# Optimization experiments

Hardware: AMD Instinct MI355X
Metric: run time of the kernel (lower is better)

Reference implementation:

```python
import jax, jax.numpy as jnp
import numpy as np

S, B, H, NH = 2048, 2, 1024, 16
DH = H // NH

def setup_inputs() -> dict:
    key = jax.random.key(0)
    ks = jax.random.split(key, 4)
    x = jax.random.normal(ks[0], (S, B, H), dtype=jnp.float32)
    attention_mask = jnp.ones((B, 1, S, S), dtype=bool)
    rotary_pos_emb = jax.random.uniform(ks[1], (S, 1, 1, DH), dtype=jnp.float32)
    Wqkv = jax.random.normal(ks[2], (H, 3 * H), dtype=jnp.float32) * (1.0 / np.sqrt(H))
    bqkv = jnp.zeros((3 * H,), dtype=jnp.float32)
    Wproj = jax.random.normal(ks[3], (H, H), dtype=jnp.float32) * (1.0 / np.sqrt(H))
    bproj = jnp.zeros((H,), dtype=jnp.float32)
    return {"x": x, "attention_mask": attention_mask, "rotary_pos_emb": rotary_pos_emb,
            "Wqkv": Wqkv, "bqkv": bqkv, "Wproj": Wproj, "bproj": bproj}

def reference(x, attention_mask, rotary_pos_emb, Wqkv, bqkv, Wproj, bproj):
    s, b, h = x.shape
    dh = h // NH
    # QKV projection; per-head layout [s,b,NH,3*dh] then split (matches view+chunk)
    qkv = (x @ Wqkv + bqkv).reshape(s, b, NH, 3 * dh)
    q, k, v = jnp.split(qkv, 3, axis=-1)  # each [s,b,NH,dh]
    # RoPE (non-interleaved, rot_dim == head_dim)
    cos = jnp.cos(rotary_pos_emb)  # [s,1,1,dh]
    sin = jnp.sin(rotary_pos_emb)
    def rope(t):
        t1, t2 = jnp.split(t, 2, axis=-1)
        return t * cos + jnp.concatenate((-t2, t1), axis=-1) * sin
    q = rope(q)
    k = rope(k)
    scale = 1.0 / np.sqrt(dh).astype(np.float32)
    # scores: [b,NH,t,s]
    scores = jnp.einsum('tbhd,sbhd->bhts', q, k) * scale
    scores = jnp.where(attention_mask, scores, jnp.float32(-1e9))
    attn = jax.nn.softmax(scores, axis=-1)
    out = jnp.einsum('bhts,sbhd->tbhd', attn, v).reshape(s, b, h)
    return out @ Wproj + bproj
```

## Files before the change

### kernel.cpp

```cpp
#include <hip/hip_runtime.h>
#include <hip/hip_bf16.h>

typedef __attribute__((ext_vector_type(8))) short bf16x8;
typedef __attribute__((ext_vector_type(4))) float f32x4;
typedef __attribute__((ext_vector_type(16))) float f32x16;
typedef __attribute__((ext_vector_type(4))) unsigned short u16x4;

#define S_LEN 2048
#define BATCH 2
#define NHEAD 16
#define DHEAD 64
#define HD    1024
#define MROWS 4096
#define NQKV  3072
#define NBH   32
#define KSPLIT 2
#define KSEG  (S_LEN / KSPLIT)


static __device__ __forceinline__ unsigned short f2bf(float f) {
  union { float f; unsigned u; } v; v.f = f;
  unsigned r = v.u + 0x7FFFu + ((v.u >> 16) & 1u);
  return (unsigned short)(r >> 16);
}
static __device__ __forceinline__ float bf2f(unsigned short h) {
  union { unsigned u; float f; } v; v.u = ((unsigned)h) << 16;
  return v.f;
}
static __device__ __forceinline__ unsigned cvt_pk(float a, float b) {
  unsigned r;
  asm("v_cvt_pk_bf16_f32 %0, %1, %2" : "=v"(r) : "v"(a), "v"(b));
  return r;
}
static __device__ __forceinline__ float exp2_hw(float x) {
  float r;
  asm("v_exp_f32 %0, %1" : "=v"(r) : "v"(x));
  return r;
}

static __device__ __forceinline__ void gl_lds16(const void* g, void* l) {
  __builtin_amdgcn_global_load_lds(
      (__attribute__((address_space(1))) void*)g,
      (__attribute__((address_space(3))) void*)l, 16, 0, 0);
}


static __device__ __forceinline__ void cvt_body(const float* __restrict__ x,
                                                unsigned short* __restrict__ Xfm,
                                                int mt, int kp, char* lmem) {
  float (*ltile)[36] = reinterpret_cast<float(*)[36]>(lmem);
  int t = threadIdx.x;
  int r = t >> 3, c4 = t & 7;
  const float* src = x + (size_t)(mt * 64 + r) * HD + kp * 32 + c4 * 4;
  float4 v0 = *reinterpret_cast<const float4*>(src);
  float4 v1 = *reinterpret_cast<const float4*>(src + (size_t)32 * HD);
  *reinterpret_cast<float4*>(&ltile[r][c4 * 4]) = v0;
  *reinterpret_cast<float4*>(&ltile[r + 32][c4 * 4]) = v1;
  __syncthreads();
  int rowin = ((t >> 6) << 4) + (t & 15), ch = (t >> 4) & 3;
  bf16x8 o;
#pragma unroll
  for (int e = 0; e < 8; ++e) o[e] = (short)f2bf(ltile[rowin][ch * 8 + e]);
  *reinterpret_cast<bf16x8*>(Xfm + (((size_t)mt * 32 + kp) * 256 + t) * 8) = o;
}

static __device__ __forceinline__ void transw_body(const float* __restrict__ W,
                                                   unsigned short* __restrict__ Wt,
                                                   int K, int N, int nt, int kb,
                                                   char* lmem) {
  unsigned short (*tile)[72] = reinterpret_cast<unsigned short(*)[72]>(lmem);
  int n0 = nt * 64, k0 = kb * 64;
  int t = threadIdx.x;
  int r  = t >> 2;
  int c4 = (t & 3) * 16;
  const float* src = W + (size_t)(k0 + r) * N + n0 + c4;
#pragma unroll
  for (int j = 0; j < 16; j += 4) {
    float4 v = *reinterpret_cast<const float4*>(src + j);
    tile[r][c4 + j + 0] = f2bf(v.x);
    tile[r][c4 + j + 1] = f2bf(v.y);
    tile[r][c4 + j + 2] = f2bf(v.z);
    tile[r][c4 + j + 3] = f2bf(v.w);
  }
  __syncthreads();
  int rowin = ((t >> 6) << 4) + (t & 15), ch = (t >> 4) & 3;
  int KP = K >> 5;
#pragma unroll
  for (int p = 0; p < 2; ++p) {
    bf16x8 o;
#pragma unroll
    for (int e = 0; e < 8; ++e) o[e] = (short)tile[p * 32 + ch * 8 + e][rowin];
    *reinterpret_cast<bf16x8*>(Wt + (((size_t)nt * KP + (k0 >> 5) + p) * 256 + t) * 8) = o;
  }
}

__global__ void k_prep(const float* __restrict__ x, unsigned short* __restrict__ Xfm,
                       const float* __restrict__ Wq, unsigned short* __restrict__ Wqt,
                       const float* __restrict__ Wp, unsigned short* __restrict__ Wpt) {
  __shared__ __align__(16) char lmem[9216];
  int id = blockIdx.x;
  if (id < 768) {
    transw_body(Wq, Wqt, HD, NQKV, id % 48, id / 48, lmem);
  } else if (id < 1024) {
    int j = id - 768;
    transw_body(Wp, Wpt, HD, HD, j % 16, j / 16, lmem);
  } else {
    int j = id - 1024;
    cvt_body(x, Xfm, j >> 5, j & 31, lmem);
  }
}

template <int OUT_BF16, int BN>
__global__ void __launch_bounds__(256)
k_gemm(const unsigned short* __restrict__ A, const unsigned short* __restrict__ Bt,
       const float* __restrict__ bias, void* __restrict__ Cout, int M, int N, int K) {
  constexpr int NF = BN / 32;
  __shared__ unsigned short As[128 * 32];
  __shared__ unsigned short Bs[BN * 32];
  int t = threadIdx.x;
  int lane = t & 63;
  int w = t >> 6;
  int g = lane >> 4, i = lane & 15;
  int wr = w >> 1, wc = w & 1;
  int bx = blockIdx.x, by = blockIdx.y;

  f32x4 acc[4][NF] = {};

  const size_t tstride = (size_t)K * 64;
  const unsigned short* a_s0 = A  + (size_t)(2 * by) * tstride + t * 8;
  const unsigned short* a_s1 = a_s0 + tstride;
  const unsigned short* b_s0 = Bt + (size_t)(bx * (BN / 64)) * tstride + t * 8;
  const unsigned short* b_s1 = b_s0 + tstride;
  unsigned short* a_d0 = &As[t * 8];
  unsigned short* a_d1 = &As[(256 + t) * 8];
  unsigned short* b_d0 = &Bs[t * 8];
  unsigned short* b_d1 = &Bs[(256 + t) * 8];

  for (int kt = 0; kt < K; kt += 32) {
    size_t koff = (size_t)kt * 64;
    __syncthreads();
    gl_lds16(a_s0 + koff, a_d0);
    gl_lds16(a_s1 + koff, a_d1);
    gl_lds16(b_s0 + koff, b_d0);
    if constexpr (BN == 128) gl_lds16(b_s1 + koff, b_d1);
    __syncthreads();

    bf16x8 af[4], bf[NF];
#pragma unroll
    for (int m = 0; m < 4; ++m)
      af[m] = *reinterpret_cast<const bf16x8*>(&As[(wr * 256 + m * 64 + lane) * 8]);
#pragma unroll
    for (int n = 0; n < NF; ++n)
      bf[n] = *reinterpret_cast<const bf16x8*>(&Bs[((wc * NF + n) * 64 + lane) * 8]);
#pragma unroll
    for (int m = 0; m < 4; ++m)
#pragma unroll
      for (int n = 0; n < NF; ++n)
        acc[m][n] = __builtin_amdgcn_mfma_f32_16x16x32_bf16(af[m], bf[n], acc[m][n], 0, 0, 0);
  }

  int crow0 = by * 128 + wr * 64;
  int ccol0 = bx * BN + wc * (BN / 2);
#pragma unroll
  for (int n = 0; n < NF; ++n) {
    int col = ccol0 + n * 16 + i;
    float bv = bias[col];
#pragma unroll
    for (int m = 0; m < 4; ++m) {
#pragma unroll
      for (int r = 0; r < 4; ++r) {
        int row = crow0 + m * 16 + g * 4 + r;
        float v = acc[m][n][r] + bv;
        if (OUT_BF16)
          reinterpret_cast<unsigned short*>(Cout)[(size_t)row * N + col] = f2bf(v);
        else
          reinterpret_cast<float*>(Cout)[(size_t)row * N + col] = v;
      }
    }
  }
}

__global__ void k_rope(const unsigned short* __restrict__ QKV, const float* __restrict__ rot,
                       unsigned short* __restrict__ Qg, unsigned short* __restrict__ Kg,
                       unsigned short* __restrict__ Vg) {
  __shared__ unsigned short vtile[32][72];
  int s0 = blockIdx.x * 32;
  int bh = blockIdx.y;
  int b = bh >> 4, nh = bh & 15;
  int t = threadIdx.x;
  int c  = t & 31;
  int hi = (t >> 5) & 1;
  int ks = t >> 6;
  int d0 = ks * 16 + hi * 8;
  int s = s0 + c;
  const unsigned short* base = QKV + ((size_t)s * BATCH + b) * NQKV + nh * 192;

  float cs[8], sn[8];
#pragma unroll
  for (int j = 0; j < 8; j += 4) {
    float4 rv = *reinterpret_cast<const float4*>(rot + (size_t)s * DHEAD + d0 + j);
    cs[j + 0] = cosf(rv.x); sn[j + 0] = sinf(rv.x);
    cs[j + 1] = cosf(rv.y); sn[j + 1] = sinf(rv.y);
    cs[j + 2] = cosf(rv.z); sn[j + 2] = sinf(rv.z);
    cs[j + 3] = cosf(rv.w); sn[j + 3] = sinf(rv.w);
  }
  float sgn = (d0 < 32) ? -1.f : 1.f;
  bf16x8 qv = *reinterpret_cast<const bf16x8*>(base + d0);
  bf16x8 qp = *reinterpret_cast<const bf16x8*>(base + (d0 ^ 32));
  bf16x8 kv = *reinterpret_cast<const bf16x8*>(base + 64 + d0);
  bf16x8 kp = *reinterpret_cast<const bf16x8*>(base + 64 + (d0 ^ 32));
  bf16x8 qo, ko;
#pragma unroll
  for (int j = 0; j < 8; ++j) {
    float q = bf2f((unsigned short)qv[j]) * cs[j] + sgn * bf2f((unsigned short)qp[j]) * sn[j];
    float k = bf2f((unsigned short)kv[j]) * cs[j] + sgn * bf2f((unsigned short)kp[j]) * sn[j];
    qo[j] = (short)f2bf(q * 0.18033688f);
    ko[j] = (short)f2bf(k);
  }
  size_t blk = ((size_t)bh * (S_LEN / 32) + (s0 >> 5)) * 2048;
  *reinterpret_cast<bf16x8*>(Qg + blk + t * 8) = qo;
  *reinterpret_cast<bf16x8*>(Kg + blk + t * 8) = ko;

  bf16x8 vv = *reinterpret_cast<const bf16x8*>(base + 128 + d0);
  *reinterpret_cast<bf16x8*>(&vtile[c][d0]) = vv;
  __syncthreads();
  int vbr = t >> 7, h = (t >> 6) & 1, hi2 = (t >> 5) & 1, cc = t & 31;
  int d = 32 * h + cc;
  bf16x8 vo;
#pragma unroll
  for (int j = 0; j < 8; ++j) vo[j] = (short)vtile[vbr * 16 + hi2 * 8 + j][d];
  size_t vblk = ((size_t)bh * (S_LEN / 16) + (s0 >> 4) + vbr) * 1024;
  *reinterpret_cast<bf16x8*>(Vg + vblk + (t & 127) * 8) = vo;
}


static __device__ __forceinline__ void sm_pv(const f32x16& sc, const bf16x8* vfr,
                                             float& l_acc, f32x16& o0, f32x16& o1) {
  float p[16];
#pragma unroll
  for (int r = 0; r < 16; ++r) p[r] = exp2_hw(sc[r]);
  float s0 = (p[0] + p[1]) + (p[2] + p[3]);
  float s1 = (p[4] + p[5]) + (p[6] + p[7]);
  float s2 = (p[8] + p[9]) + (p[10] + p[11]);
  float s3 = (p[12] + p[13]) + (p[14] + p[15]);
  l_acc += (s0 + s1) + (s2 + s3);
#pragma unroll
  for (int ksl = 0; ksl < 2; ++ksl) {
    unsigned A0 = cvt_pk(p[8 * ksl + 0], p[8 * ksl + 1]);
    unsigned A1 = cvt_pk(p[8 * ksl + 2], p[8 * ksl + 3]);
    unsigned A2 = cvt_pk(p[8 * ksl + 4], p[8 * ksl + 5]);
    unsigned A3 = cvt_pk(p[8 * ksl + 6], p[8 * ksl + 7]);
    asm volatile("v_permlane32_swap_b32 %0, %1" : "+v"(A0), "+v"(A2));
    asm volatile("v_permlane32_swap_b32 %0, %1" : "+v"(A1), "+v"(A3));
    union { unsigned u[4]; bf16x8 v; } pa;
    pa.u[0] = A0; pa.u[1] = A1; pa.u[2] = A2; pa.u[3] = A3;
    __builtin_amdgcn_s_setprio(1);
    o0 = __builtin_amdgcn_mfma_f32_32x32x16_bf16(pa.v, vfr[2 * ksl + 0], o0, 0, 0, 0);
    o1 = __builtin_amdgcn_mfma_f32_32x32x16_bf16(pa.v, vfr[2 * ksl + 1], o1, 0, 0, 0);
    __builtin_amdgcn_s_setprio(0);
  }
}

__global__ void __launch_bounds__(256, 2)
k_flash(const unsigned short* __restrict__ Qg, const unsigned short* __restrict__ Kg,
        const unsigned short* __restrict__ Vg, unsigned short* __restrict__ Opart,
        float* __restrict__ Lpart) {
  __shared__ unsigned short kv_lds[2 * 8192];
  int bh = blockIdx.x, qt = blockIdx.y, kv = blockIdx.z;
  int t = threadIdx.x, lane = t & 63;
  int c = lane & 31, hi = lane >> 5;

  int q0 = qt * 128 + (t >> 6) * 32;
  int kv0 = kv * KSEG;
  const unsigned short* Qb = Qg + (size_t)bh * S_LEN * DHEAD + (size_t)q0 * DHEAD;
  const unsigned short* Kb = Kg + (size_t)bh * S_LEN * DHEAD;
  const unsigned short* Vb = Vg + (size_t)bh * S_LEN * DHEAD;

  bf16x8 qf[4];
#pragma unroll
  for (int ks = 0; ks < 4; ++ks)
    qf[ks] = *reinterpret_cast<const bf16x8*>(Qb + ((size_t)ks * 64 + lane) * 8);

#define STAGE(kt, bufi) do {                                                   \
    const unsigned short* _ks = Kb + (size_t)(kt) * DHEAD;                     \
    const unsigned short* _vs = Vb + (size_t)(kt) * DHEAD;                     \
    unsigned short* _kd = &kv_lds[(bufi) * 8192];                              \
    unsigned short* _vd = _kd + 4096;                                          \
    gl_lds16(_ks + t * 8, _kd + t * 8);                                        \
    gl_lds16(_ks + (t + 256) * 8, _kd + (t + 256) * 8);                        \
    gl_lds16(_vs + t * 8, _vd + t * 8);                                        \
    gl_lds16(_vs + (t + 256) * 8, _vd + (t + 256) * 8);                        \
  } while (0)

  f32x16 o0 = {}, o1 = {};
  float l_acc = 0.f;
  int cur = 0;

  STAGE(kv0, 0);
  for (int kt = kv0; kt < kv0 + KSEG; kt += 64) {
    __syncthreads();
    int nxt = kv0 + (((kt - kv0) + 64) & (KSEG - 1));
    STAGE(nxt, cur ^ 1);

    const unsigned short* kbuf = &kv_lds[cur * 8192];
    const unsigned short* vbuf = kbuf + 4096;

    f32x16 scA = {}, scB = {};
    __builtin_amdgcn_s_setprio(1);
#pragma unroll
    for (int ks = 0; ks < 4; ++ks) {
      bf16x8 kf = *reinterpret_cast<const bf16x8*>(kbuf + (ks * 64 + lane) * 8);
      scA = __builtin_amdgcn_mfma_f32_32x32x16_bf16(kf, qf[ks], scA, 0, 0, 0);
    }
#pragma unroll
    for (int ks = 0; ks < 4; ++ks) {
      bf16x8 kf = *reinterpret_cast<const bf16x8*>(kbuf + (256 + ks * 64 + lane) * 8);
      scB = __builtin_amdgcn_mfma_f32_32x32x16_bf16(kf, qf[ks], scB, 0, 0, 0);
    }
    __builtin_amdgcn_s_setprio(0);

    bf16x8 va[4], vb[4];
#pragma unroll
    for (int g = 0; g < 2; ++g) {
      va[2 * g + 0] = *reinterpret_cast<const bf16x8*>(vbuf + (g * 128 + lane) * 8);
      va[2 * g + 1] = *reinterpret_cast<const bf16x8*>(vbuf + (g * 128 + 64 + lane) * 8);
      vb[2 * g + 0] = *reinterpret_cast<const bf16x8*>(vbuf + ((g + 2) * 128 + lane) * 8);
      vb[2 * g + 1] = *reinterpret_cast<const bf16x8*>(vbuf + ((g + 2) * 128 + 64 + lane) * 8);
    }

    sm_pv(scA, va, l_acc, o0, o1);
    sm_pv(scB, vb, l_acc, o0, o1);
    cur ^= 1;
  }
#undef STAGE

  float l_tot = l_acc + __shfl_xor(l_acc, 32, 64);

  unsigned short* Op = Opart + ((size_t)kv * NBH + bh) * S_LEN * DHEAD;
  if (hi == 0) Lpart[((size_t)kv * NBH + bh) * S_LEN + q0 + c] = l_tot;
#pragma unroll
  for (int r = 0; r < 16; ++r) {
    int crow = (r & 3) + 8 * (r >> 2) + 4 * hi;
    size_t rowoff = (size_t)(q0 + crow) * DHEAD;
    Op[rowoff + c]      = f2bf(o0[r]);
    Op[rowoff + 32 + c] = f2bf(o1[r]);
  }
}

__global__ void k_reduce(const unsigned short* __restrict__ Op, const float* __restrict__ Lp,
                         unsigned short* __restrict__ Afm) {
  __shared__ unsigned short lds[64][72];
  const int kvO = NBH * S_LEN * DHEAD;
  const int kvL = NBH * S_LEN;
  int mt = blockIdx.x, nh = blockIdx.y;
  int t = threadIdx.x;
  int lq = (t >> 3) & 31, gd = t & 7;
  int qg = mt * 32 + lq;

  bf16x8 gr[4];
#pragma unroll
  for (int kvb = 0; kvb < 4; ++kvb) {
    int kv = kvb >> 1, b = kvb & 1;
    gr[kvb] = *reinterpret_cast<const bf16x8*>(
        Op + (size_t)kv * kvO + ((size_t)(b * 16 + nh) * S_LEN + qg) * DHEAD + gd * 8);
  }
#pragma unroll
  for (int b = 0; b < 2; ++b) {
    size_t li = (size_t)(b * 16 + nh) * S_LEN + qg;
    float inv = 1.0f / (Lp[li] + Lp[kvL + li]);
    bf16x8 o;
#pragma unroll
    for (int e = 0; e < 8; ++e)
      o[e] = (short)f2bf((bf2f((unsigned short)gr[b][e]) +
                          bf2f((unsigned short)gr[2 + b][e])) * inv);
    *reinterpret_cast<bf16x8*>(&lds[b * 32 + lq][gd * 8]) = o;
  }
  __syncthreads();

  int rowin = ((t >> 6) << 4) + (t & 15), ch = (t >> 4) & 3;
  int lr = (rowin & 1) * 32 + (rowin >> 1);
#pragma unroll
  for (int p = 0; p < 2; ++p) {
    bf16x8 o = *reinterpret_cast<const bf16x8*>(&lds[lr][p * 32 + ch * 8]);
    *reinterpret_cast<bf16x8*>(Afm + (((size_t)mt * 32 + nh * 2 + p) * 256 + t) * 8) = o;
  }
}

extern "C" void kernel_launch(void* const* d_in, const int* in_sizes, int n_in,
                              void* d_out, int out_size, void* d_ws, size_t ws_size,
                              hipStream_t stream) {
  const float* x     = (const float*)d_in[0];
  const float* rot   = (const float*)d_in[2];
  const float* Wqkv  = (const float*)d_in[3];
  const float* bqkv  = (const float*)d_in[4];
  const float* Wproj = (const float*)d_in[5];
  const float* bproj = (const float*)d_in[6];
  float* out = (float*)d_out;

  char* ws = (char*)d_ws;
  unsigned short* xb   = (unsigned short*)(ws);
  unsigned short* Wqt  = (unsigned short*)(ws + 8388608);
  unsigned short* Wpt  = (unsigned short*)(ws + 14680064);
  unsigned short* QKV  = (unsigned short*)(ws + 16777216);
  unsigned short* Qs   = (unsigned short*)(ws + 41943040);
  unsigned short* Kst  = (unsigned short*)(ws + 50331648);
  unsigned short* Vtt  = (unsigned short*)(ws + 58720256);
  unsigned short* Opart = (unsigned short*)(ws + 16777216);
  float*          Lpart = (float*)(ws + 33554432);
  unsigned short* attn  = xb;

  k_prep<<<3072, 256, 0, stream>>>(x, xb, Wqkv, Wqt, Wproj, Wpt);
  k_gemm<1, 128><<<dim3(NQKV / 128, MROWS / 128), 256, 0, stream>>>(xb, Wqt, bqkv, QKV,
                                                                    MROWS, NQKV, HD);
  k_rope<<<dim3(S_LEN / 32, BATCH * NHEAD), 256, 0, stream>>>(QKV, rot, Qs, Kst, Vtt);
  k_flash<<<dim3(NBH, S_LEN / 128, KSPLIT), 256, 0, stream>>>(Qs, Kst, Vtt, Opart, Lpart);
  k_reduce<<<dim3(MROWS / 64, NHEAD), 256, 0, stream>>>(Opart, Lpart, attn);
  k_gemm<0, 64><<<dim3(HD / 64, MROWS / 128), 256, 0, stream>>>(attn, Wpt, bproj, out,
                                                                MROWS, HD, HD);
}
```

Before: 129.1 us.

## Fuse split-KV reduction into output projection GEMM A-tile load

Removes the separate k_reduce kernel and has the output projection GEMM combine the two KV-split partial outputs and normalize by the summed softmax denominators while loading each A tile into LDS. This saves one kernel launch and the round trip of the combined attention tensor through global memory. In exchange, each of the 16 column blocks recomputes the reduction for its row tile, the A loads become register-staged instead of direct-to-LDS, and the new GEMM has no visible software pipelining, which may cost compute efficiency.

```diff
diff --git a/kernel.cpp b/kernel.cpp
--- a/kernel.cpp
+++ b/kernel.cpp
@@ -43,7 +43,6 @@
       (__attribute__((address_space(1))) void*)g,
       (__attribute__((address_space(3))) void*)l, 16, 0, 0);
 }
-
 
 static __device__ __forceinline__ void cvt_body(const float* __restrict__ x,
                                                 unsigned short* __restrict__ Xfm,
@@ -180,6 +179,97 @@
   }
 }
 
+__global__ void __launch_bounds__(256)
+k_gemm2f(const unsigned short* __restrict__ Op, const float* __restrict__ Lp,
+         const unsigned short* __restrict__ Bt, const float* __restrict__ bias,
+         float* __restrict__ Cout) {
+  constexpr int K = HD, N = HD;
+  const int kvO = NBH * S_LEN * DHEAD;
+  const int kvL = NBH * S_LEN;
+  __shared__ unsigned short As[128 * 32];
+  __shared__ unsigned short Bs[64 * 32];
+  int t = threadIdx.x;
+  int lane = t & 63;
+  int w = t >> 6;
+  int g = lane >> 4, i = lane & 15;
+  int wr = w >> 1, wc = w & 1;
+  int bx = blockIdx.x, by = blockIdx.y;
+
+  f32x4 acc[4][2] = {};
+
+  const size_t tstride = (size_t)K * 64;
+  const unsigned short* b_s0 = Bt + (size_t)bx * tstride + t * 8;
+
+  int rowin = ((t >> 6) << 4) + (t & 15);
+  int ch = (t >> 4) & 3;
+  int r0 = by * 128 + rowin;
+  int r1 = r0 + 64;
+  int q0 = r0 >> 1, b0 = r0 & 1;
+  int q1 = r1 >> 1, b1 = r1 & 1;
+
+  for (int kt = 0; kt < K; kt += 32) {
+    size_t koff = (size_t)kt * 64;
+    __syncthreads();
+    gl_lds16(b_s0 + koff, &Bs[t * 8]);
+    int nh = kt >> 6;
+    int d = (kt & 63) + ch * 8;
+    {
+      size_t li = (size_t)(b0 * 16 + nh) * S_LEN + q0;
+      float inv = 1.0f / (Lp[li] + Lp[kvL + li]);
+      bf16x8 g0 = *reinterpret_cast<const bf16x8*>(Op + li * DHEAD + d);
+      bf16x8 g1 = *reinterpret_cast<const bf16x8*>(Op + (size_t)kvO + li * DHEAD + d);
+      bf16x8 o;
+#pragma unroll
+      for (int e = 0; e < 8; ++e)
+        o[e] = (short)f2bf((bf2f((unsigned short)g0[e]) +
+                            bf2f((unsigned short)g1[e])) * inv);
+      *reinterpret_cast<bf16x8*>(&As[t * 8]) = o;
+    }
+    {
+      size_t li = (size_t)(b1 * 16 + nh) * S_LEN + q1;
+      float inv = 1.0f / (Lp[li] + Lp[kvL + li]);
+      bf16x8 g0 = *reinterpret_cast<const bf16x8*>(Op + li * DHEAD + d);
+      bf16x8 g1 = *reinterpret_cast<const bf16x8*>(Op + (size_t)kvO + li * DHEAD + d);
+      bf16x8 o;
+#pragma unroll
+      for (int e = 0; e < 8; ++e)
+        o[e] = (short)f2bf((bf2f((unsigned short)g0[e]) +
+                            bf2f((unsigned short)g1[e])) * inv);
+      *reinterpret_cast<bf16x8*>(&As[(256 + t) * 8]) = o;
+    }
+    __syncthreads();
+
+    bf16x8 af[4], bf[2];
+#pragma unroll
+    for (int m = 0; m < 4; ++m)
+      af[m] = *reinterpret_cast<const bf16x8*>(&As[(wr * 256 + m * 64 + lane) * 8]);
+#pragma unroll
+    for (int n = 0; n < 2; ++n)
+      bf[n] = *reinterpret_cast<const bf16x8*>(&Bs[((wc * 2 + n) * 64 + lane) * 8]);
+#pragma unroll
+    for (int m = 0; m < 4; ++m)
+#pragma unroll
+      for (int n = 0; n < 2; ++n)
+        acc[m][n] = __builtin_amdgcn_mfma_f32_16x16x32_bf16(af[m], bf[n], acc[m][n], 0, 0, 0);
+  }
+
+  int crow0 = by * 128 + wr * 64;
+  int ccol0 = bx * 64 + wc * 32;
+#pragma unroll
+  for (int n = 0; n < 2; ++n) {
+    int col = ccol0 + n * 16 + i;
+    float bv = bias[col];
+#pragma unroll
+    for (int m = 0; m < 4; ++m) {
+#pragma unroll
+      for (int r = 0; r < 4; ++r) {
+        int row = crow0 + m * 16 + g * 4 + r;
+        Cout[(size_t)row * N + col] = acc[m][n][r] + bv;
+      }
+    }
+  }
+}
+
 __global__ void k_rope(const unsigned short* __restrict__ QKV, const float* __restrict__ rot,
                        unsigned short* __restrict__ Qg, unsigned short* __restrict__ Kg,
                        unsigned short* __restrict__ Vg) {
@@ -233,7 +323,6 @@
   *reinterpret_cast<bf16x8*>(Vg + vblk + (t & 127) * 8) = vo;
 }
 
-
 static __device__ __forceinline__ void sm_pv(const f32x16& sc, const bf16x8* vfr,
                                              float& l_acc, f32x16& o0, f32x16& o1) {
   float p[16];
@@ -347,45 +436,6 @@
   }
 }
 
-__global__ void k_reduce(const unsigned short* __restrict__ Op, const float* __restrict__ Lp,
-                         unsigned short* __restrict__ Afm) {
-  __shared__ unsigned short lds[64][72];
-  const int kvO = NBH * S_LEN * DHEAD;
-  const int kvL = NBH * S_LEN;
-  int mt = blockIdx.x, nh = blockIdx.y;
-  int t = threadIdx.x;
-  int lq = (t >> 3) & 31, gd = t & 7;
-  int qg = mt * 32 + lq;
-
-  bf16x8 gr[4];
-#pragma unroll
-  for (int kvb = 0; kvb < 4; ++kvb) {
-    int kv = kvb >> 1, b = kvb & 1;
-    gr[kvb] = *reinterpret_cast<const bf16x8*>(
-        Op + (size_t)kv * kvO + ((size_t)(b * 16 + nh) * S_LEN + qg) * DHEAD + gd * 8);
-  }
-#pragma unroll
-  for (int b = 0; b < 2; ++b) {
-    size_t li = (size_t)(b * 16 + nh) * S_LEN + qg;
-    float inv = 1.0f / (Lp[li] + Lp[kvL + li]);
-    bf16x8 o;
-#pragma unroll
-    for (int e = 0; e < 8; ++e)
-      o[e] = (short)f2bf((bf2f((unsigned short)gr[b][e]) +
-                          bf2f((unsigned short)gr[2 + b][e])) * inv);
-    *reinterpret_cast<bf16x8*>(&lds[b * 32 + lq][gd * 8]) = o;
-  }
-  __syncthreads();
-
-  int rowin = ((t >> 6) << 4) + (t & 15), ch = (t >> 4) & 3;
-  int lr = (rowin & 1) * 32 + (rowin >> 1);
-#pragma unroll
-  for (int p = 0; p < 2; ++p) {
-    bf16x8 o = *reinterpret_cast<const bf16x8*>(&lds[lr][p * 32 + ch * 8]);
-    *reinterpret_cast<bf16x8*>(Afm + (((size_t)mt * 32 + nh * 2 + p) * 256 + t) * 8) = o;
-  }
-}
-
 extern "C" void kernel_launch(void* const* d_in, const int* in_sizes, int n_in,
                               void* d_out, int out_size, void* d_ws, size_t ws_size,
                               hipStream_t stream) {
@@ -407,14 +457,11 @@
   unsigned short* Vtt  = (unsigned short*)(ws + 58720256);
   unsigned short* Opart = (unsigned short*)(ws + 16777216);
   float*          Lpart = (float*)(ws + 33554432);
-  unsigned short* attn  = xb;
 
   k_prep<<<3072, 256, 0, stream>>>(x, xb, Wqkv, Wqt, Wproj, Wpt);
   k_gemm<1, 128><<<dim3(NQKV / 128, MROWS / 128), 256, 0, stream>>>(xb, Wqt, bqkv, QKV,
                                                                     MROWS, NQKV, HD);
   k_rope<<<dim3(S_LEN / 32, BATCH * NHEAD), 256, 0, stream>>>(QKV, rot, Qs, Kst, Vtt);
   k_flash<<<dim3(NBH, S_LEN / 128, KSPLIT), 256, 0, stream>>>(Qs, Kst, Vtt, Opart, Lpart);
-  k_reduce<<<dim3(MROWS / 64, NHEAD), 256, 0, stream>>>(Opart, Lpart, attn);
-  k_gemm<0, 64><<<dim3(HD / 64, MROWS / 128), 256, 0, stream>>>(attn, Wpt, bproj, out,
-                                                                MROWS, HD, HD);
-}
+  k_gemm2f<<<dim3(HD / 64, MROWS / 128), 256, 0, stream>>>(Opart, Lpart, Wpt, bproj, out);
+}
```

Result: slower. 157.4 us (+21.9%).
